# Kernel tuning notes

Measured on AMD Instinct MI355X. Metric: run time of the kernel, lower is better.

Reference implementation:

```python
import jax, jax.numpy as jnp
import numpy as np

GATE_SLOPE = 10.0
ALPHA = 0.8
STRIDE = 1
PADDING = 1


def _unfold(x, kH, kW, stride, padding):
    # torch F.unfold equivalent, kept as (B, Cin, kH, kW, Hout, Wout)
    B, C, H, W = x.shape
    xp = jnp.pad(x, ((0, 0), (0, 0), (padding, padding), (padding, padding)))
    Hout = (H + 2 * padding - kH) // stride + 1
    Wout = (W + 2 * padding - kW) // stride + 1
    cols = []
    for i in range(kH):          # small fixed loop over kernel taps (9 iters)
        for j in range(kW):
            cols.append(xp[:, :, i:i + Hout * stride:stride, j:j + Wout * stride:stride])
    return jnp.stack(cols, axis=2).reshape(B, C, kH, kW, Hout, Wout)


def setup_inputs() -> dict:
    key = jax.random.key(0)
    ks = jax.random.split(key, 6)
    B, Cin, H, W = 4, 16, 32, 32
    Cout, K, kH, kW = 32, 3, 3, 3
    pshape = (Cout, Cin, K, kH, kW)
    x = jax.random.normal(ks[0], (B, Cin, H, W), jnp.float32)
    k = jax.random.uniform(ks[1], pshape, jnp.float32) * 2.0 + 0.5
    Ec = jax.random.uniform(ks[2], pshape, jnp.float32) * 2.0 + 0.5
    Ps = jax.random.uniform(ks[3], pshape, jnp.float32) * 1.5 + 0.5
    bias = jax.random.normal(ks[4], pshape, jnp.float32) * 0.1
    coef = jax.random.normal(ks[5], pshape, jnp.float32)
    out_bias = jnp.zeros((Cout,), jnp.float32)
    return {"x": x, "k": k, "Ec": Ec, "Ps": Ps, "bias": bias, "coef": coef, "out_bias": out_bias}


def reference(x, k, Ec, Ps, bias, coef, out_bias):
    kH, kW = k.shape[-2], k.shape[-1]
    patches = _unfold(x, kH, kW, STRIDE, PADDING)          # (B,Cin,kH,kW,Hout,Wout)
    # broadcast layout: (B, Cout, Cin, K, kH, kW, Hout, Wout)
    xe = patches[:, None, :, None]                          # (B,1,Cin,1,kH,kW,Ho,Wo)
    def bc(p):
        return p[None, :, :, :, :, :, None, None]
    k_, Ec_, Ps_, b_, c_ = bc(k), bc(Ec), bc(Ps), bc(bias), bc(coef)
    # stateless mode: prev_x = detach(x_exp) -> dx == 0 in value, grad flows via xe
    prev_x = jax.lax.stop_gradient(xe)
    is_moving_up = jax.nn.sigmoid(GATE_SLOPE * (xe - prev_x))
    crossed_pos = jax.nn.sigmoid(GATE_SLOPE * (xe - Ec_))
    crossed_neg = jax.nn.sigmoid(GATE_SLOPE * (-xe - Ec_))
    su = is_moving_up * crossed_pos
    sl = (1.0 - is_moving_up) * crossed_neg
    # branch_prev = +1 (stateless)
    target_sign = su - sl + (1.0 - su - sl)
    branch_mom = ALPHA + (1.0 - ALPHA) * target_sign
    shifted_x = xe + Ec_ * branch_mom
    basis = Ps_ * jnp.tanh(k_ * shifted_x) + b_
    out = jnp.sum(basis * c_, axis=(2, 3, 4, 5))            # (B,Cout,Hout,Wout)
    return out + out_bias[None, :, None, None]
```

## Files before the change

kernel.cpp:

```cpp
#include <hip/hip_runtime.h>


#define LOG2E 1.4426950408889634f

__global__ __launch_bounds__(256, 4) void ferro_main(
    const float* __restrict__ x,
    const float* __restrict__ k, const float* __restrict__ Ec,
    const float* __restrict__ Ps, const float* __restrict__ bias,
    const float* __restrict__ coef, const float* __restrict__ out_bias,
    float* __restrict__ out)
{
    const int bid = blockIdx.x;
    const int rs  = bid & 7;
    const int co  = (bid >> 3) & 31;
    const int b   = bid >> 8;
    const int tid = threadIdx.x;

    __shared__ float4 p4s[432];
    __shared__ float  pAs[432];
    __shared__ float  xs[16 * 6 * 34];
    __shared__ float  red[4];
    __shared__ float  csh;

    const int pbase = co * 432;
    float cpart = 0.f;
    for (int s = tid; s < 432; s += 256) {
        float kv = k[pbase + s];
        float ev = Ec[pbase + s];
        float pv = Ps[pbase + s];
        float bv = bias[pbase + s];
        float cv = coef[pbase + s];
        float G  = 2.f * LOG2E * kv;
        float4 v;
        v.x = -10.f * LOG2E * ev;
        v.y = G;
        v.z = 0.8f * G * ev;
        v.w = 0.2f * G * ev;
        int cin = s / 27;
        int r   = s - cin * 27;
        int kk  = r / 9;
        int ij  = r - kk * 9;
        int dst = cin * 27 + ij * 3 + kk;
        p4s[dst] = v;
        pAs[dst] = -2.f * pv * cv;
        cpart += (pv + bv) * cv;
    }

    const int r0 = rs * 4;
    const float* xb = x + b * (16 * 1024);
    for (int idx = tid; idx < 16 * 204; idx += 256) {
        int cin  = idx / 204;
        int rem  = idx - cin * 204;
        int row6 = rem / 34;
        int colp = rem - row6 * 34;
        int gr = r0 + row6 - 1;
        int gc = colp - 1;
        float v = 0.f;
        if ((unsigned)gr < 32u && (unsigned)gc < 32u)
            v = xb[(cin * 32 + gr) * 32 + gc];
        xs[idx] = v;
    }

    #pragma unroll
    for (int off = 32; off > 0; off >>= 1)
        cpart += __shfl_down(cpart, off, 64);
    if ((tid & 63) == 0) red[tid >> 6] = cpart;
    __syncthreads();
    if (tid == 0) csh = red[0] + red[1] + red[2] + red[3];
    __syncthreads();

    const int lane = tid & 63;
    const int w    = tid >> 6;
    const int col  = lane & 31;
    const int cinh = lane >> 5;
    const float Cx = -10.f * LOG2E;
    float acc0 = 0.f, acc1 = 0.f, acc2 = 0.f;

    #pragma unroll 1
    for (int c8 = 0; c8 < 8; ++c8) {
        const int cin = cinh * 8 + c8;
        const float*  xr = &xs[cin * 204 + w * 34 + col];
        const float4* pp = &p4s[cin * 27];
        const float*  aa = &pAs[cin * 27];
        #pragma unroll
        for (int ij = 0; ij < 9; ++ij) {
            const int i = ij / 3, j = ij - (ij / 3) * 3;
            float xv = xr[i * 34 + j];
            float xC = Cx * xv;
            {
                float4 v  = pp[ij * 3 + 0];
                float e1 = __builtin_amdgcn_exp2f(xC + v.x);
                float s  = __builtin_amdgcn_rcpf(e1 + 1.f);
                float e2 = __builtin_amdgcn_exp2f(fmaf(v.w, s, fmaf(v.y, xv, v.z)));
                float u  = __builtin_amdgcn_rcpf(e2 + 1.f);
                acc0 = fmaf(aa[ij * 3 + 0], u, acc0);
            }
            {
                float4 v  = pp[ij * 3 + 1];
                float e1 = __builtin_amdgcn_exp2f(xC + v.x);
                float s  = __builtin_amdgcn_rcpf(e1 + 1.f);
                float e2 = __builtin_amdgcn_exp2f(fmaf(v.w, s, fmaf(v.y, xv, v.z)));
                float u  = __builtin_amdgcn_rcpf(e2 + 1.f);
                acc1 = fmaf(aa[ij * 3 + 1], u, acc1);
            }
            {
                float4 v  = pp[ij * 3 + 2];
                float e1 = __builtin_amdgcn_exp2f(xC + v.x);
                float s  = __builtin_amdgcn_rcpf(e1 + 1.f);
                float e2 = __builtin_amdgcn_exp2f(fmaf(v.w, s, fmaf(v.y, xv, v.z)));
                float u  = __builtin_amdgcn_rcpf(e2 + 1.f);
                acc2 = fmaf(aa[ij * 3 + 2], u, acc2);
            }
        }
    }

    float acc = (acc0 + acc1) + acc2;
    acc += __shfl_xor(acc, 32, 64);
    if (cinh == 0) {
        out[((b * 32 + co) * 32 + (r0 + w)) * 32 + col] = acc + csh + out_bias[co];
    }
}

extern "C" void kernel_launch(void* const* d_in, const int* in_sizes, int n_in,
                              void* d_out, int out_size, void* d_ws, size_t ws_size,
                              hipStream_t stream) {
    const float* x        = (const float*)d_in[0];
    const float* k        = (const float*)d_in[1];
    const float* Ec       = (const float*)d_in[2];
    const float* Ps       = (const float*)d_in[3];
    const float* bias     = (const float*)d_in[4];
    const float* coef     = (const float*)d_in[5];
    const float* out_bias = (const float*)d_in[6];
    float* out = (float*)d_out;

    ferro_main<<<dim3(1024), dim3(256), 0, stream>>>(
        x, k, Ec, Ps, bias, coef, out_bias, out);
}
```

Baseline: 91.64 us.

## Split work across more blocks with two rows and cin quarters, fold coef into float4

Each block now covers two output rows instead of four, and warps split the 16 input channels into quarters, so the grid doubles to 2048 blocks with higher occupancy bounds. The partial sums per channel group are combined through a shared-memory reduction before the store. The per-tap parameter pack is reorganised so the Ps*coef weight sits in the float4's w slot, which removes the separate pAs array and its load. This adds a __syncthreads and redoes the parameter precompute and halo loads in twice as many blocks.

New measurement: 91.18 us. No clear change (-0.5%).

```diff
diff --git a/kernel.cpp b/kernel.cpp
--- a/kernel.cpp
+++ b/kernel.cpp
@@ -3,7 +3,7 @@
 
 #define LOG2E 1.4426950408889634f
 
-__global__ __launch_bounds__(256, 4) void ferro_main(
+__global__ __launch_bounds__(256, 8) void ferro_main(
     const float* __restrict__ x,
     const float* __restrict__ k, const float* __restrict__ Ec,
     const float* __restrict__ Ps, const float* __restrict__ bias,
@@ -11,15 +11,15 @@
     float* __restrict__ out)
 {
     const int bid = blockIdx.x;
-    const int rs  = bid & 7;
-    const int co  = (bid >> 3) & 31;
-    const int b   = bid >> 8;
+    const int rs  = bid & 15;
+    const int co  = (bid >> 4) & 31;
+    const int b   = bid >> 9;
     const int tid = threadIdx.x;
 
     __shared__ float4 p4s[432];
-    __shared__ float  pAs[432];
-    __shared__ float  xs[16 * 6 * 34];
-    __shared__ float  red[4];
+    __shared__ float  xs[16 * 4 * 34];
+    __shared__ float  red[128];
+    __shared__ float  redc[4];
     __shared__ float  csh;
 
     const int pbase = co * 432;
@@ -30,30 +30,27 @@
         float pv = Ps[pbase + s];
         float bv = bias[pbase + s];
         float cv = coef[pbase + s];
-        float G  = 2.f * LOG2E * kv;
         float4 v;
         v.x = -10.f * LOG2E * ev;
-        v.y = G;
-        v.z = 0.8f * G * ev;
-        v.w = 0.2f * G * ev;
+        v.y = 2.f * LOG2E * kv;
+        v.z = 0.8f * ev;
+        v.w = -2.f * pv * cv;
         int cin = s / 27;
         int r   = s - cin * 27;
         int kk  = r / 9;
         int ij  = r - kk * 9;
-        int dst = cin * 27 + ij * 3 + kk;
-        p4s[dst] = v;
-        pAs[dst] = -2.f * pv * cv;
+        p4s[cin * 27 + ij * 3 + kk] = v;
         cpart += (pv + bv) * cv;
     }
 
-    const int r0 = rs * 4;
+    const int r0 = rs * 2;
     const float* xb = x + b * (16 * 1024);
-    for (int idx = tid; idx < 16 * 204; idx += 256) {
-        int cin  = idx / 204;
-        int rem  = idx - cin * 204;
-        int row6 = rem / 34;
-        int colp = rem - row6 * 34;
-        int gr = r0 + row6 - 1;
+    for (int idx = tid; idx < 16 * 136; idx += 256) {
+        int cin  = idx / 136;
+        int rem  = idx - cin * 136;
+        int row4 = rem / 34;
+        int colp = rem - row4 * 34;
+        int gr = r0 + row4 - 1;
         int gc = colp - 1;
         float v = 0.f;
         if ((unsigned)gr < 32u && (unsigned)gc < 32u)
@@ -64,60 +61,72 @@
     #pragma unroll
     for (int off = 32; off > 0; off >>= 1)
         cpart += __shfl_down(cpart, off, 64);
-    if ((tid & 63) == 0) red[tid >> 6] = cpart;
+    if ((tid & 63) == 0) redc[tid >> 6] = cpart;
     __syncthreads();
-    if (tid == 0) csh = red[0] + red[1] + red[2] + red[3];
+    if (tid == 0) csh = redc[0] + redc[1] + redc[2] + redc[3];
     __syncthreads();
 
     const int lane = tid & 63;
     const int w    = tid >> 6;
+    const int row  = w >> 1;
+    const int cinq = w & 1;
     const int col  = lane & 31;
     const int cinh = lane >> 5;
     const float Cx = -10.f * LOG2E;
     float acc0 = 0.f, acc1 = 0.f, acc2 = 0.f;
 
+    const int cinbase = cinq * 8 + cinh * 4;
     #pragma unroll 1
-    for (int c8 = 0; c8 < 8; ++c8) {
-        const int cin = cinh * 8 + c8;
-        const float*  xr = &xs[cin * 204 + w * 34 + col];
+    for (int c = 0; c < 4; ++c) {
+        const int cin = cinbase + c;
+        const float*  xr = &xs[cin * 136 + row * 34 + col];
         const float4* pp = &p4s[cin * 27];
-        const float*  aa = &pAs[cin * 27];
         #pragma unroll
         for (int ij = 0; ij < 9; ++ij) {
             const int i = ij / 3, j = ij - (ij / 3) * 3;
             float xv = xr[i * 34 + j];
             float xC = Cx * xv;
             {
-                float4 v  = pp[ij * 3 + 0];
+                float4 v = pp[ij * 3 + 0];
                 float e1 = __builtin_amdgcn_exp2f(xC + v.x);
                 float s  = __builtin_amdgcn_rcpf(e1 + 1.f);
-                float e2 = __builtin_amdgcn_exp2f(fmaf(v.w, s, fmaf(v.y, xv, v.z)));
+                float sh = fmaf(v.z, fmaf(0.25f, s, 1.f), xv);
+                float e2 = __builtin_amdgcn_exp2f(v.y * sh);
                 float u  = __builtin_amdgcn_rcpf(e2 + 1.f);
-                acc0 = fmaf(aa[ij * 3 + 0], u, acc0);
+                acc0 = fmaf(v.w, u, acc0);
             }
             {
-                float4 v  = pp[ij * 3 + 1];
+                float4 v = pp[ij * 3 + 1];
                 float e1 = __builtin_amdgcn_exp2f(xC + v.x);
                 float s  = __builtin_amdgcn_rcpf(e1 + 1.f);
-                float e2 = __builtin_amdgcn_exp2f(fmaf(v.w, s, fmaf(v.y, xv, v.z)));
+                float sh = fmaf(v.z, fmaf(0.25f, s, 1.f), xv);
+                float e2 = __builtin_amdgcn_exp2f(v.y * sh);
                 float u  = __builtin_amdgcn_rcpf(e2 + 1.f);
-                acc1 = fmaf(aa[ij * 3 + 1], u, acc1);
+                acc1 = fmaf(v.w, u, acc1);
             }
             {
-                float4 v  = pp[ij * 3 + 2];
+                float4 v = pp[ij * 3 + 2];
                 float e1 = __builtin_amdgcn_exp2f(xC + v.x);
                 float s  = __builtin_amdgcn_rcpf(e1 + 1.f);
-                float e2 = __builtin_amdgcn_exp2f(fmaf(v.w, s, fmaf(v.y, xv, v.z)));
+                float sh = fmaf(v.z, fmaf(0.25f, s, 1.f), xv);
+                float e2 = __builtin_amdgcn_exp2f(v.y * sh);
                 float u  = __builtin_amdgcn_rcpf(e2 + 1.f);
-                acc2 = fmaf(aa[ij * 3 + 2], u, acc2);
+                acc2 = fmaf(v.w, u, acc2);
             }
         }
     }
 
     float acc = (acc0 + acc1) + acc2;
     acc += __shfl_xor(acc, 32, 64);
-    if (cinh == 0) {
-        out[((b * 32 + co) * 32 + (r0 + w)) * 32 + col] = acc + csh + out_bias[co];
+    if (cinh == 0) red[w * 32 + col] = acc;
+    __syncthreads();
+
+    if (tid < 64) {
+        int r   = tid >> 5;
+        int cl  = tid & 31;
+        float v = red[(r * 2 + 0) * 32 + cl] + red[(r * 2 + 1) * 32 + cl]
+                + csh + out_bias[co];
+        out[((b * 32 + co) * 32 + (r0 + r)) * 32 + cl] = v;
     }
 }
 
@@ -133,6 +142,6 @@
     const float* out_bias = (const float*)d_in[6];
     float* out = (float*)d_out;
 
-    ferro_main<<<dim3(1024), dim3(256), 0, stream>>>(
+    ferro_main<<<dim3(2048), dim3(256), 0, stream>>>(
         x, k, Ec, Ps, bias, coef, out_bias, out);
 }
```
